# Kernel tuning notes

Hardware: AMD Instinct MI355X
Metric: run time of the kernel (lower is better)

The kernel has to match this reference:

```python
import jax, jax.numpy as jnp
import numpy as np

B, S, D = 2, 2048, 1024
H, HD = 16, 64  # num_attention_heads, attention_head_size


def setup_inputs() -> dict:
    key = jax.random.key(0)
    ks = jax.random.split(key, 8)
    std = 0.02
    return {
        "hidden_states": jax.random.normal(ks[0], (B, S, D), dtype=jnp.float32),
        "attention_mask": jnp.zeros((B, 1, 1, S), dtype=jnp.float32),
        "Wq": jax.random.normal(ks[1], (D, D), dtype=jnp.float32) * std,
        "bq": jnp.zeros((D,), dtype=jnp.float32),
        "Wk": jax.random.normal(ks[2], (D, D), dtype=jnp.float32) * std,
        "bk": jnp.zeros((D,), dtype=jnp.float32),
        "Wv": jax.random.normal(ks[3], (D, D), dtype=jnp.float32) * std,
        "bv": jnp.zeros((D,), dtype=jnp.float32),
    }


def reference(hidden_states, attention_mask, Wq, bq, Wk, bk, Wv, bv):
    b, s, d = hidden_states.shape

    def split_heads(x):  # [b,s,D] -> [b,H,s,HD]
        return x.reshape(b, s, H, HD).transpose(0, 2, 1, 3)

    q = split_heads(hidden_states @ Wq + bq)
    k = split_heads(hidden_states @ Wk + bk)
    v = split_heads(hidden_states @ Wv + bv)

    scores = jnp.einsum("bhqd,bhkd->bhqk", q, k) / jnp.sqrt(jnp.float32(HD))
    scores = scores + attention_mask  # additive mask, broadcast [b,1,1,s]
    probs = jax.nn.softmax(scores, axis=-1)  # dropout is identity at inference
    ctx = jnp.einsum("bhqk,bhkd->bhqd", probs, v)
    out = ctx.transpose(0, 2, 1, 3).reshape(b, s, d)
    return out
```

## Files before the change

### kernel.cpp

```cpp
#include <hip/hip_runtime.h>
#include <math.h>

#define CB 2
#define CS 2048
#define CD 1024
#define CH 16
#define CHD 64
#define CM (CB*CS)

#define QSCALE 0.18033688f
#define LOG2E  1.44269504f
#define BLOG   40.0f

typedef unsigned short u16;
using bf16x8 = __attribute__((ext_vector_type(8))) short;
using u16x8  = __attribute__((ext_vector_type(8))) unsigned short;
using f32x4  = __attribute__((ext_vector_type(4))) float;

__device__ __forceinline__ u16 f2bf(float f) {
    unsigned int u = __float_as_uint(f);
    u = (u + 0x7FFFu + ((u >> 16) & 1u)) >> 16;
    return (u16)u;
}

__device__ __forceinline__ unsigned pack2bf(float a, float b) {
    unsigned ua = (__float_as_uint(a) + 0x8000u) >> 16;
    unsigned ub = (__float_as_uint(b) + 0x8000u) & 0xFFFF0000u;
    return ua | ub;
}

__device__ __forceinline__ void load_lds16(const u16* g, u16* l) {
    __builtin_amdgcn_global_load_lds(
        (const __attribute__((address_space(1))) unsigned int*)g,
        (__attribute__((address_space(3))) unsigned int*)l, 16, 0, 0);
}

__global__ __launch_bounds__(256)
void convert_x(const float* __restrict__ X, u16* __restrict__ Xb)
{
    size_t i = ((size_t)blockIdx.x * 256 + threadIdx.x) * 8;
    float4 v0 = *(const float4*)(X + i);
    float4 v1 = *(const float4*)(X + i + 4);
    u16x8 o;
    o[0] = f2bf(v0.x); o[1] = f2bf(v0.y); o[2] = f2bf(v0.z); o[3] = f2bf(v0.w);
    o[4] = f2bf(v1.x); o[5] = f2bf(v1.y); o[6] = f2bf(v1.z); o[7] = f2bf(v1.w);
    *(u16x8*)(Xb + i) = o;
}

__global__ __launch_bounds__(256)
void convert_wt(const float* __restrict__ Wq, const float* __restrict__ Wk,
                const float* __restrict__ Wv, u16* __restrict__ Wt)
{
    const int z = blockIdx.z;
    const float* W = (z == 0) ? Wq : (z == 1) ? Wk : Wv;
    const float sc = (z == 0) ? QSCALE : 1.0f;
    u16* Wo = Wt + (size_t)z * CD * CD;

    __shared__ u16 T[64][72];
    const int k0 = blockIdx.x << 6;
    const int n0 = blockIdx.y << 6;
    const int tid = threadIdx.x;

    #pragma unroll
    for (int it = 0; it < 4; ++it) {
        int r = (tid >> 4) + (it << 4);
        int c = (tid & 15) << 2;
        float4 v = *(const float4*)(W + (size_t)(k0 + r) * CD + n0 + c);
        T[c + 0][r] = f2bf(v.x * sc);
        T[c + 1][r] = f2bf(v.y * sc);
        T[c + 2][r] = f2bf(v.z * sc);
        T[c + 3][r] = f2bf(v.w * sc);
    }
    __syncthreads();
    #pragma unroll
    for (int it = 0; it < 2; ++it) {
        int cc = tid + (it << 8);
        int n  = cc >> 3;
        int ch = (cc & 7) << 3;
        *(uint4*)(Wo + (size_t)(n0 + n) * CD + k0 + ch) = *(const uint4*)&T[n][ch];
    }
}

__global__ __launch_bounds__(256, 3)
void qkv_gemm_mfma(const u16* __restrict__ Xb, const u16* __restrict__ Wt,
                   const float* __restrict__ bq, const float* __restrict__ bk,
                   const float* __restrict__ bv,
                   u16* __restrict__ Qb, u16* __restrict__ Kb,
                   u16* __restrict__ Vt)
{
    const int z = blockIdx.z;
    const u16* W = Wt + (size_t)z * CD * CD;
    const float* bias = (z == 0) ? bq : (z == 1) ? bk : bv;
    const float bscale = (z == 0) ? QSCALE : 1.0f;

    __shared__ u16 smem[16384];
    u16* As = smem;
    u16* Bs = smem + 8192;

    const int tid  = threadIdx.x;
    const int w    = tid >> 6;
    const int l    = tid & 63;
    const int l15  = l & 15;
    const int quad = l >> 4;
    const int wm   = w >> 1;
    const int wn   = w & 1;

    const int row0 = blockIdx.x << 7;
    const int n0   = blockIdx.y << 7;

    f32x4 acc[4][4];
    #pragma unroll
    for (int mi = 0; mi < 4; ++mi)
        #pragma unroll
        for (int nt = 0; nt < 4; ++nt)
            acc[mi][nt] = (f32x4){0.f, 0.f, 0.f, 0.f};

    const u16* Ag = Xb + (size_t)row0 * CD;
    const u16* Bg = W  + (size_t)n0   * CD;
    const int lr8 = l >> 3;
    const int ls  = l & 7;
    const int lg  = (ls ^ lr8) << 3;
    const int q7  = l15 & 7;

    for (int k0 = 0; k0 < CD; k0 += 64) {
        __syncthreads();
        #pragma unroll
        for (int i = 0; i < 4; ++i) {
            int r = w * 32 + 8 * i + lr8;
            load_lds16(Ag + (size_t)r * CD + k0 + lg, As + (size_t)(w * 32 + 8 * i) * 64);
            load_lds16(Bg + (size_t)r * CD + k0 + lg, Bs + (size_t)(w * 32 + 8 * i) * 64);
        }
        __syncthreads();

        #pragma unroll
        for (int kk = 0; kk < 2; ++kk) {
            bf16x8 af[4], bfr[4];
            #pragma unroll
            for (int mi = 0; mi < 4; ++mi)
                af[mi] = *(const bf16x8*)
                    &As[(wm * 64 + mi * 16 + l15) * 64 + (((kk * 4 + quad) ^ q7) << 3)];
            #pragma unroll
            for (int nt = 0; nt < 4; ++nt)
                bfr[nt] = *(const bf16x8*)
                    &Bs[(wn * 64 + nt * 16 + l15) * 64 + (((kk * 4 + quad) ^ q7) << 3)];
            #pragma unroll
            for (int mi = 0; mi < 4; ++mi)
                #pragma unroll
                for (int nt = 0; nt < 4; ++nt)
                    acc[mi][nt] = __builtin_amdgcn_mfma_f32_16x16x32_bf16(
                        af[mi], bfr[nt], acc[mi][nt], 0, 0, 0);
        }
    }

    __syncthreads();

    if (z < 2) {
        u16* Og = (z == 0) ? Qb : Kb;
        float bb[4];
        #pragma unroll
        for (int nt = 0; nt < 4; ++nt)
            bb[nt] = bias[n0 + wn * 64 + nt * 16 + l15] * bscale;

        u16 (*Ct)[136] = (u16(*)[136])smem;
        #pragma unroll
        for (int mh = 0; mh < 2; ++mh) {
            if (wm == mh) {
                #pragma unroll
                for (int nt = 0; nt < 4; ++nt)
                    #pragma unroll
                    for (int mi = 0; mi < 4; ++mi)
                        #pragma unroll
                        for (int r = 0; r < 4; ++r)
                            Ct[mi * 16 + quad * 4 + r][wn * 64 + nt * 16 + l15] =
                                f2bf(acc[mi][nt][r] + bb[nt]);
            }
            __syncthreads();
            #pragma unroll
            for (int it = 0; it < 4; ++it) {
                int c  = tid + (it << 8);
                int rl = c >> 4;
                int ck = c & 15;
                uint4 d = *(const uint4*)&Ct[rl][ck * 8];
                int gcol = n0 + ck * 8;
                int h = gcol >> 6, hd = gcol & 63;
                int m = row0 + mh * 64 + rl;
                int b = m >> 11, s = m & (CS - 1);
                *(uint4*)(Og + ((size_t)(b * CH + h) * CS + s) * CHD + hd) = d;
            }
            __syncthreads();
        }
    } else {
        u16 (*Ct)[136] = (u16(*)[136])smem;
        #pragma unroll
        for (int nh = 0; nh < 2; ++nh) {
            if (wn == nh) {
                #pragma unroll
                for (int nt = 0; nt < 4; ++nt) {
                    int col = n0 + nh * 64 + nt * 16 + l15;
                    float bb = bias[col];
                    #pragma unroll
                    for (int mi = 0; mi < 4; ++mi)
                        #pragma unroll
                        for (int r = 0; r < 4; ++r) {
                            int ml = wm * 64 + mi * 16 + quad * 4 + r;
                            Ct[nt * 16 + l15][ml] = f2bf(acc[mi][nt][r] + bb);
                        }
                }
            }
            __syncthreads();
            #pragma unroll
            for (int it = 0; it < 4; ++it) {
                int c   = tid + (it << 8);
                int dvl = c >> 4;
                int ch  = c & 15;
                uint4 vdat = *(const uint4*)&Ct[dvl][ch * 8];
                int col = n0 + nh * 64 + dvl;
                int h   = col >> 6;
                int dv  = col & 63;
                int m0  = row0 + ch * 8;
                int b   = m0 >> 11;
                int s0  = m0 & (CS - 1);
                *(uint4*)(Vt + (((size_t)(b * CH + h)) * CHD + dv) * CS + s0) = vdat;
            }
            __syncthreads();
        }
    }
}

__global__ __launch_bounds__(256, 2)
void attn_mfma(const u16* __restrict__ Qg, const u16* __restrict__ Kg,
               const u16* __restrict__ Vtg, const float* __restrict__ mask,
               float* __restrict__ out)
{
    __shared__ float msk[CS];
    __shared__ u16   Kst[2][64 * 64];
    __shared__ u16   Vst[2][64 * 64];
    __shared__ u16   Pl[4][32 * 64];
    __shared__ float abuf[4][32];

    const int q0  = blockIdx.x << 7;
    const int bh  = blockIdx.y;
    const int b   = bh >> 4;
    const int h   = bh & 15;
    const int tid = threadIdx.x;
    const int w    = tid >> 6;
    const int l    = tid & 63;
    const int l15  = l & 15;
    const int quad = l >> 4;
    const int q7   = l15 & 7;
    const int lr8  = l >> 3;
    const int lg   = ((l & 7) ^ lr8) << 3;

    const u16* Qp = Qg  + (size_t)bh * CS * CHD;
    const u16* Kp = Kg  + (size_t)bh * CS * CHD;
    const u16* Vp = Vtg + (size_t)bh * CHD * CS;
    const float* mrow = mask + (size_t)b * CS;

    {
        int i = tid * 8;
        float4 a = *(const float4*)(mrow + i);
        float4 c = *(const float4*)(mrow + i + 4);
        msk[i + 0] = a.x * LOG2E - BLOG; msk[i + 1] = a.y * LOG2E - BLOG;
        msk[i + 2] = a.z * LOG2E - BLOG; msk[i + 3] = a.w * LOG2E - BLOG;
        msk[i + 4] = c.x * LOG2E - BLOG; msk[i + 5] = c.y * LOG2E - BLOG;
        msk[i + 6] = c.z * LOG2E - BLOG; msk[i + 7] = c.w * LOG2E - BLOG;
    }

    auto stage = [&](int k0, int bb) {
        #pragma unroll
        for (int i = 0; i < 2; ++i) {
            int rl = w * 16 + 8 * i;
            load_lds16(Kp + (size_t)(k0 + rl + lr8) * CHD + lg, &Kst[bb][rl * 64]);
            load_lds16(Vp + (size_t)(rl + lr8) * CS + k0 + lg,  &Vst[bb][rl * 64]);
        }
    };

    stage(0, 0);

    bf16x8 qf[2][2];
    #pragma unroll
    for (int nq = 0; nq < 2; ++nq)
        #pragma unroll
        for (int hh = 0; hh < 2; ++hh)
            qf[nq][hh] = *(const bf16x8*)(
                Qp + (size_t)(q0 + w * 32 + nq * 16 + l15) * CHD + hh * 32 + quad * 8);

    u16* Pw = &Pl[w][0];
    float lsum[2] = {0.f, 0.f};
    f32x4 O[2][4];
    #pragma unroll
    for (int nq = 0; nq < 2; ++nq)
        #pragma unroll
        for (int dt = 0; dt < 4; ++dt)
            O[nq][dt] = (f32x4){0.f, 0.f, 0.f, 0.f};

    for (int kt = 0; kt < CS / 64; ++kt) {
        const int k0 = kt << 6;
        const int cc = kt & 1;
        __syncthreads();
        if (kt + 1 < CS / 64)
            stage(k0 + 64, cc ^ 1);

        bf16x8 kf[4][2];
        #pragma unroll
        for (int mt = 0; mt < 4; ++mt)
            #pragma unroll
            for (int hh = 0; hh < 2; ++hh)
                kf[mt][hh] = *(const bf16x8*)
                    &Kst[cc][(mt * 16 + l15) * 64 + (((hh * 4 + quad) ^ q7) << 3)];

        #pragma unroll
        for (int nq = 0; nq < 2; ++nq) {
            f32x4 st[4];
            #pragma unroll
            for (int mt = 0; mt < 4; ++mt) {
                f32x4 c0 = *(const f32x4*)&msk[k0 + mt * 16 + quad * 4];
                c0 = __builtin_amdgcn_mfma_f32_16x16x32_bf16(kf[mt][0], qf[nq][0], c0, 0, 0, 0);
                st[mt] = __builtin_amdgcn_mfma_f32_16x16x32_bf16(kf[mt][1], qf[nq][1], c0, 0, 0, 0);
            }
            float rs = lsum[nq];
            #pragma unroll
            for (int mt = 0; mt < 4; ++mt) {
                #pragma unroll
                for (int r = 0; r < 4; ++r) {
                    st[mt][r] = exp2f(st[mt][r]);
                    rs += st[mt][r];
                }
                int g = 2 * mt + (quad >> 1);
                int addr = (nq * 16 + l15) * 64 + ((g ^ q7) << 3) + ((quad & 1) << 2);
                uint2 d;
                d.x = pack2bf(st[mt][0], st[mt][1]);
                d.y = pack2bf(st[mt][2], st[mt][3]);
                *(uint2*)&Pw[addr] = d;
            }
            lsum[nq] = rs;
        }

        bf16x8 pf[2][2];
        #pragma unroll
        for (int nq = 0; nq < 2; ++nq)
            #pragma unroll
            for (int hh = 0; hh < 2; ++hh)
                pf[nq][hh] = *(const bf16x8*)
                    &Pw[(nq * 16 + l15) * 64 + (((hh * 4 + quad) ^ q7) << 3)];

        bf16x8 vf[4][2];
        #pragma unroll
        for (int dt = 0; dt < 4; ++dt)
            #pragma unroll
            for (int hh = 0; hh < 2; ++hh)
                vf[dt][hh] = *(const bf16x8*)
                    &Vst[cc][(dt * 16 + l15) * 64 + (((hh * 4 + quad) ^ q7) << 3)];

        #pragma unroll
        for (int nq = 0; nq < 2; ++nq)
            #pragma unroll
            for (int dt = 0; dt < 4; ++dt) {
                O[nq][dt] = __builtin_amdgcn_mfma_f32_16x16x32_bf16(
                    pf[nq][0], vf[dt][0], O[nq][dt], 0, 0, 0);
                O[nq][dt] = __builtin_amdgcn_mfma_f32_16x16x32_bf16(
                    pf[nq][1], vf[dt][1], O[nq][dt], 0, 0, 0);
            }
    }

    #pragma unroll
    for (int nq = 0; nq < 2; ++nq) {
        lsum[nq] += __shfl_xor(lsum[nq], 16);
        lsum[nq] += __shfl_xor(lsum[nq], 32);
    }
    if (quad == 0) {
        abuf[w][l15]      = lsum[0];
        abuf[w][16 + l15] = lsum[1];
    }
    __builtin_amdgcn_s_waitcnt(0);

    #pragma unroll
    for (int nq = 0; nq < 2; ++nq) {
        f32x4 lo = *(const f32x4*)&abuf[w][nq * 16 + quad * 4];
        #pragma unroll
        for (int r = 0; r < 4; ++r) {
            float inv = 1.0f / lo[r];
            int q = q0 + w * 32 + nq * 16 + quad * 4 + r;
            float* orow = out + ((size_t)b * CS + q) * CD + h * CHD;
            #pragma unroll
            for (int dt = 0; dt < 4; ++dt)
                orow[dt * 16 + l15] = O[nq][dt][r] * inv;
        }
    }
}

extern "C" void kernel_launch(void* const* d_in, const int* in_sizes, int n_in,
                              void* d_out, int out_size, void* d_ws, size_t ws_size,
                              hipStream_t stream)
{
    const float* X    = (const float*)d_in[0];
    const float* mask = (const float*)d_in[1];
    const float* Wq   = (const float*)d_in[2];
    const float* bq   = (const float*)d_in[3];
    const float* Wk   = (const float*)d_in[4];
    const float* bk   = (const float*)d_in[5];
    const float* Wv   = (const float*)d_in[6];
    const float* bv   = (const float*)d_in[7];
    float* out = (float*)d_out;

    char* ws = (char*)d_ws;
    u16* Xb = (u16*)(ws);
    u16* Wt = (u16*)(ws + ((size_t)8  << 20));
    u16* Qb = (u16*)(ws + ((size_t)14 << 20));
    u16* Kb = (u16*)(ws + ((size_t)22 << 20));
    u16* Vt = (u16*)(ws + ((size_t)30 << 20));

    convert_x<<<CM * CD / (256 * 8), 256, 0, stream>>>(X, Xb);
    convert_wt<<<dim3(16, 16, 3), 256, 0, stream>>>(Wq, Wk, Wv, Wt);
    qkv_gemm_mfma<<<dim3(CM / 128, CD / 128, 3), 256, 0, stream>>>(
        Xb, Wt, bq, bk, bv, Qb, Kb, Vt);
    attn_mfma<<<dim3(CS / 128, CB * CH), 256, 0, stream>>>(Qb, Kb, Vt, mask, out);
}
```

Baseline: 194.7 us.

## Shrink GEMM and attention tiles to raise occupancy and block count

The QKV GEMM tile goes from 128x128 to 128x64 output, with the grid reordered so blocks sharing a row panel of X are adjacent, and launch bounds raised. The attention kernel drops from 128 to 64 queries per block (16 per wave), removes K/V double buffering and the LDS row-sum buffer, and targets 4 blocks per CU. Smaller tiles cut register and LDS use so more waves can run, but they add load traffic per FLOP and remove the prefetch overlap in attention.

```diff
diff --git a/kernel.cpp b/kernel.cpp
--- a/kernel.cpp
+++ b/kernel.cpp
@@ -81,7 +81,7 @@
     }
 }
 
-__global__ __launch_bounds__(256, 3)
+__global__ __launch_bounds__(256, 6)
 void qkv_gemm_mfma(const u16* __restrict__ Xb, const u16* __restrict__ Wt,
                    const float* __restrict__ bq, const float* __restrict__ bk,
                    const float* __restrict__ bv,
@@ -93,7 +93,7 @@
     const float* bias = (z == 0) ? bq : (z == 1) ? bk : bv;
     const float bscale = (z == 0) ? QSCALE : 1.0f;
 
-    __shared__ u16 smem[16384];
+    __shared__ u16 smem[12288];
     u16* As = smem;
     u16* Bs = smem + 8192;
 
@@ -105,140 +105,123 @@
     const int wm   = w >> 1;
     const int wn   = w & 1;
 
-    const int row0 = blockIdx.x << 7;
-    const int n0   = blockIdx.y << 7;
-
-    f32x4 acc[4][4];
+    const int n0   = blockIdx.x << 6;
+    const int row0 = blockIdx.y << 7;
+
+    f32x4 acc[4][2];
     #pragma unroll
     for (int mi = 0; mi < 4; ++mi)
         #pragma unroll
-        for (int nt = 0; nt < 4; ++nt)
+        for (int nt = 0; nt < 2; ++nt)
             acc[mi][nt] = (f32x4){0.f, 0.f, 0.f, 0.f};
 
     const u16* Ag = Xb + (size_t)row0 * CD;
     const u16* Bg = W  + (size_t)n0   * CD;
     const int lr8 = l >> 3;
-    const int ls  = l & 7;
-    const int lg  = (ls ^ lr8) << 3;
+    const int lg  = ((l & 7) ^ lr8) << 3;
     const int q7  = l15 & 7;
 
     for (int k0 = 0; k0 < CD; k0 += 64) {
         __syncthreads();
         #pragma unroll
         for (int i = 0; i < 4; ++i) {
-            int r = w * 32 + 8 * i + lr8;
-            load_lds16(Ag + (size_t)r * CD + k0 + lg, As + (size_t)(w * 32 + 8 * i) * 64);
-            load_lds16(Bg + (size_t)r * CD + k0 + lg, Bs + (size_t)(w * 32 + 8 * i) * 64);
+            int r = w * 32 + 8 * i;
+            load_lds16(Ag + (size_t)(r + lr8) * CD + k0 + lg, As + (size_t)r * 64);
+        }
+        #pragma unroll
+        for (int i = 0; i < 2; ++i) {
+            int r = w * 16 + 8 * i;
+            load_lds16(Bg + (size_t)(r + lr8) * CD + k0 + lg, Bs + (size_t)r * 64);
         }
         __syncthreads();
 
         #pragma unroll
         for (int kk = 0; kk < 2; ++kk) {
-            bf16x8 af[4], bfr[4];
+            const int slot = ((kk * 4 + quad) ^ q7) << 3;
+            bf16x8 af[4], bfr[2];
             #pragma unroll
             for (int mi = 0; mi < 4; ++mi)
-                af[mi] = *(const bf16x8*)
-                    &As[(wm * 64 + mi * 16 + l15) * 64 + (((kk * 4 + quad) ^ q7) << 3)];
-            #pragma unroll
-            for (int nt = 0; nt < 4; ++nt)
-                bfr[nt] = *(const bf16x8*)
-                    &Bs[(wn * 64 + nt * 16 + l15) * 64 + (((kk * 4 + quad) ^ q7) << 3)];
+                af[mi] = *(const bf16x8*)&As[(wm * 64 + mi * 16 + l15) * 64 + slot];
+            #pragma unroll
+            for (int nt = 0; nt < 2; ++nt)
+                bfr[nt] = *(const bf16x8*)&Bs[(wn * 32 + nt * 16 + l15) * 64 + slot];
             #pragma unroll
             for (int mi = 0; mi < 4; ++mi)
                 #pragma unroll
-                for (int nt = 0; nt < 4; ++nt)
+                for (int nt = 0; nt < 2; ++nt)
                     acc[mi][nt] = __builtin_amdgcn_mfma_f32_16x16x32_bf16(
                         af[mi], bfr[nt], acc[mi][nt], 0, 0, 0);
         }
     }
 
     __syncthreads();
+    const int h = n0 >> 6;
 
     if (z < 2) {
         u16* Og = (z == 0) ? Qb : Kb;
-        float bb[4];
-        #pragma unroll
-        for (int nt = 0; nt < 4; ++nt)
-            bb[nt] = bias[n0 + wn * 64 + nt * 16 + l15] * bscale;
-
-        u16 (*Ct)[136] = (u16(*)[136])smem;
-        #pragma unroll
-        for (int mh = 0; mh < 2; ++mh) {
-            if (wm == mh) {
+        float bb[2];
+        #pragma unroll
+        for (int nt = 0; nt < 2; ++nt)
+            bb[nt] = bias[n0 + wn * 32 + nt * 16 + l15] * bscale;
+
+        u16 (*Ct)[72] = (u16(*)[72])smem;
+        #pragma unroll
+        for (int nt = 0; nt < 2; ++nt)
+            #pragma unroll
+            for (int mi = 0; mi < 4; ++mi)
                 #pragma unroll
-                for (int nt = 0; nt < 4; ++nt)
-                    #pragma unroll
-                    for (int mi = 0; mi < 4; ++mi)
-                        #pragma unroll
-                        for (int r = 0; r < 4; ++r)
-                            Ct[mi * 16 + quad * 4 + r][wn * 64 + nt * 16 + l15] =
-                                f2bf(acc[mi][nt][r] + bb[nt]);
-            }
-            __syncthreads();
-            #pragma unroll
-            for (int it = 0; it < 4; ++it) {
-                int c  = tid + (it << 8);
-                int rl = c >> 4;
-                int ck = c & 15;
-                uint4 d = *(const uint4*)&Ct[rl][ck * 8];
-                int gcol = n0 + ck * 8;
-                int h = gcol >> 6, hd = gcol & 63;
-                int m = row0 + mh * 64 + rl;
-                int b = m >> 11, s = m & (CS - 1);
-                *(uint4*)(Og + ((size_t)(b * CH + h) * CS + s) * CHD + hd) = d;
-            }
-            __syncthreads();
+                for (int r = 0; r < 4; ++r)
+                    Ct[wm * 64 + mi * 16 + quad * 4 + r][wn * 32 + nt * 16 + l15] =
+                        f2bf(acc[mi][nt][r] + bb[nt]);
+        __syncthreads();
+        #pragma unroll
+        for (int it = 0; it < 4; ++it) {
+            int c  = tid + (it << 8);
+            int rl = c >> 3;
+            int ck = c & 7;
+            uint4 d = *(const uint4*)&Ct[rl][ck * 8];
+            int m = row0 + rl;
+            int b = m >> 11, s = m & (CS - 1);
+            *(uint4*)(Og + ((size_t)(b * CH + h) * CS + s) * CHD + ck * 8) = d;
         }
     } else {
         u16 (*Ct)[136] = (u16(*)[136])smem;
         #pragma unroll
-        for (int nh = 0; nh < 2; ++nh) {
-            if (wn == nh) {
+        for (int nt = 0; nt < 2; ++nt) {
+            float bb = bias[n0 + wn * 32 + nt * 16 + l15];
+            #pragma unroll
+            for (int mi = 0; mi < 4; ++mi)
                 #pragma unroll
-                for (int nt = 0; nt < 4; ++nt) {
-                    int col = n0 + nh * 64 + nt * 16 + l15;
-                    float bb = bias[col];
-                    #pragma unroll
-                    for (int mi = 0; mi < 4; ++mi)
-                        #pragma unroll
-                        for (int r = 0; r < 4; ++r) {
-                            int ml = wm * 64 + mi * 16 + quad * 4 + r;
-                            Ct[nt * 16 + l15][ml] = f2bf(acc[mi][nt][r] + bb);
-                        }
-                }
-            }
-            __syncthreads();
-            #pragma unroll
-            for (int it = 0; it < 4; ++it) {
-                int c   = tid + (it << 8);
-                int dvl = c >> 4;
-                int ch  = c & 15;
-                uint4 vdat = *(const uint4*)&Ct[dvl][ch * 8];
-                int col = n0 + nh * 64 + dvl;
-                int h   = col >> 6;
-                int dv  = col & 63;
-                int m0  = row0 + ch * 8;
-                int b   = m0 >> 11;
-                int s0  = m0 & (CS - 1);
-                *(uint4*)(Vt + (((size_t)(b * CH + h)) * CHD + dv) * CS + s0) = vdat;
-            }
-            __syncthreads();
-        }
-    }
-}
-
-__global__ __launch_bounds__(256, 2)
+                for (int r = 0; r < 4; ++r)
+                    Ct[wn * 32 + nt * 16 + l15][wm * 64 + mi * 16 + quad * 4 + r] =
+                        f2bf(acc[mi][nt][r] + bb);
+        }
+        __syncthreads();
+        #pragma unroll
+        for (int it = 0; it < 4; ++it) {
+            int c   = tid + (it << 8);
+            int dvl = c >> 4;
+            int ch  = c & 15;
+            uint4 vdat = *(const uint4*)&Ct[dvl][ch * 8];
+            int m0 = row0 + ch * 8;
+            int b  = m0 >> 11;
+            int s0 = m0 & (CS - 1);
+            *(uint4*)(Vt + (((size_t)(b * CH + h)) * CHD + dvl) * CS + s0) = vdat;
+        }
+    }
+}
+
+__global__ __launch_bounds__(256, 4)
 void attn_mfma(const u16* __restrict__ Qg, const u16* __restrict__ Kg,
                const u16* __restrict__ Vtg, const float* __restrict__ mask,
                float* __restrict__ out)
 {
     __shared__ float msk[CS];
-    __shared__ u16   Kst[2][64 * 64];
-    __shared__ u16   Vst[2][64 * 64];
-    __shared__ u16   Pl[4][32 * 64];
-    __shared__ float abuf[4][32];
-
-    const int q0  = blockIdx.x << 7;
+    __shared__ u16   Kst[64 * 64];
+    __shared__ u16   Vst[64 * 64];
+    __shared__ u16   Pl[4][16 * 64];
+
+    const int q0  = blockIdx.x << 6;
     const int bh  = blockIdx.y;
     const int b   = bh >> 4;
     const int h   = bh & 15;
@@ -266,40 +249,28 @@
         msk[i + 6] = c.z * LOG2E - BLOG; msk[i + 7] = c.w * LOG2E - BLOG;
     }
 
-    auto stage = [&](int k0, int bb) {
+    bf16x8 qf[2];
+    #pragma unroll
+    for (int hh = 0; hh < 2; ++hh)
+        qf[hh] = *(const bf16x8*)(
+            Qp + (size_t)(q0 + w * 16 + l15) * CHD + hh * 32 + quad * 8);
+
+    u16* Pw = &Pl[w][0];
+    float lsum = 0.f;
+    f32x4 O[4];
+    #pragma unroll
+    for (int dt = 0; dt < 4; ++dt) O[dt] = (f32x4){0.f, 0.f, 0.f, 0.f};
+
+    for (int kt = 0; kt < CS / 64; ++kt) {
+        const int k0 = kt << 6;
+        __syncthreads();
         #pragma unroll
         for (int i = 0; i < 2; ++i) {
             int rl = w * 16 + 8 * i;
-            load_lds16(Kp + (size_t)(k0 + rl + lr8) * CHD + lg, &Kst[bb][rl * 64]);
-            load_lds16(Vp + (size_t)(rl + lr8) * CS + k0 + lg,  &Vst[bb][rl * 64]);
-        }
-    };
-
-    stage(0, 0);
-
-    bf16x8 qf[2][2];
-    #pragma unroll
-    for (int nq = 0; nq < 2; ++nq)
-        #pragma unroll
-        for (int hh = 0; hh < 2; ++hh)
-            qf[nq][hh] = *(const bf16x8*)(
-                Qp + (size_t)(q0 + w * 32 + nq * 16 + l15) * CHD + hh * 32 + quad * 8);
-
-    u16* Pw = &Pl[w][0];
-    float lsum[2] = {0.f, 0.f};
-    f32x4 O[2][4];
-    #pragma unroll
-    for (int nq = 0; nq < 2; ++nq)
-        #pragma unroll
-        for (int dt = 0; dt < 4; ++dt)
-            O[nq][dt] = (f32x4){0.f, 0.f, 0.f, 0.f};
-
-    for (int kt = 0; kt < CS / 64; ++kt) {
-        const int k0 = kt << 6;
-        const int cc = kt & 1;
-        __syncthreads();
-        if (kt + 1 < CS / 64)
-            stage(k0 + 64, cc ^ 1);
+            load_lds16(Kp + (size_t)(k0 + rl + lr8) * CHD + lg, &Kst[rl * 64]);
+            load_lds16(Vp + (size_t)(rl + lr8) * CS + k0 + lg,  &Vst[rl * 64]);
+        }
+        __syncthreads();
 
         bf16x8 kf[4][2];
         #pragma unroll
@@ -307,42 +278,38 @@
             #pragma unroll
             for (int hh = 0; hh < 2; ++hh)
                 kf[mt][hh] = *(const bf16x8*)
-                    &Kst[cc][(mt * 16 + l15) * 64 + (((hh * 4 + quad) ^ q7) << 3)];
-
-        #pragma unroll
-        for (int nq = 0; nq < 2; ++nq) {
-            f32x4 st[4];
-            #pragma unroll
-            for (int mt = 0; mt < 4; ++mt) {
-                f32x4 c0 = *(const f32x4*)&msk[k0 + mt * 16 + quad * 4];
-                c0 = __builtin_amdgcn_mfma_f32_16x16x32_bf16(kf[mt][0], qf[nq][0], c0, 0, 0, 0);
-                st[mt] = __builtin_amdgcn_mfma_f32_16x16x32_bf16(kf[mt][1], qf[nq][1], c0, 0, 0, 0);
+                    &Kst[(mt * 16 + l15) * 64 + (((hh * 4 + quad) ^ q7) << 3)];
+
+        f32x4 st[4];
+        #pragma unroll
+        for (int mt = 0; mt < 4; ++mt) {
+            f32x4 c0 = *(const f32x4*)&msk[k0 + mt * 16 + quad * 4];
+            c0 = __builtin_amdgcn_mfma_f32_16x16x32_bf16(kf[mt][0], qf[0], c0, 0, 0, 0);
+            st[mt] = __builtin_amdgcn_mfma_f32_16x16x32_bf16(kf[mt][1], qf[1], c0, 0, 0, 0);
+        }
+
+        float rs = lsum;
+        #pragma unroll
+        for (int mt = 0; mt < 4; ++mt) {
+            #pragma unroll
+            for (int r = 0; r < 4; ++r) {
+                st[mt][r] = exp2f(st[mt][r]);
+                rs += st[mt][r];
             }
-            float rs = lsum[nq];
-            #pragma unroll
-            for (int mt = 0; mt < 4; ++mt) {
-                #pragma unroll
-                for (int r = 0; r < 4; ++r) {
-                    st[mt][r] = exp2f(st[mt][r]);
-                    rs += st[mt][r];
-                }
-                int g = 2 * mt + (quad >> 1);
-                int addr = (nq * 16 + l15) * 64 + ((g ^ q7) << 3) + ((quad & 1) << 2);
-                uint2 d;
-                d.x = pack2bf(st[mt][0], st[mt][1]);
-                d.y = pack2bf(st[mt][2], st[mt][3]);
-                *(uint2*)&Pw[addr] = d;
-            }
-            lsum[nq] = rs;
-        }
-
-        bf16x8 pf[2][2];
-        #pragma unroll
-        for (int nq = 0; nq < 2; ++nq)
-            #pragma unroll
-            for (int hh = 0; hh < 2; ++hh)
-                pf[nq][hh] = *(const bf16x8*)
-                    &Pw[(nq * 16 + l15) * 64 + (((hh * 4 + quad) ^ q7) << 3)];
+            int g = 2 * mt + (quad >> 1);
+            int addr = l15 * 64 + ((g ^ q7) << 3) + ((quad & 1) << 2);
+            uint2 d;
+            d.x = pack2bf(st[mt][0], st[mt][1]);
+            d.y = pack2bf(st[mt][2], st[mt][3]);
+            *(uint2*)&Pw[addr] = d;
+        }
+        lsum = rs;
+
+        bf16x8 pf[2];
+        #pragma unroll
+        for (int hh = 0; hh < 2; ++hh)
+            pf[hh] = *(const bf16x8*)
+                &Pw[l15 * 64 + (((hh * 4 + quad) ^ q7) << 3)];
 
         bf16x8 vf[4][2];
         #pragma unroll
@@ -350,42 +317,26 @@
             #pragma unroll
             for (int hh = 0; hh < 2; ++hh)
                 vf[dt][hh] = *(const bf16x8*)
-                    &Vst[cc][(dt * 16 + l15) * 64 + (((hh * 4 + quad) ^ q7) << 3)];
-
-        #pragma unroll
-        for (int nq = 0; nq < 2; ++nq)
-            #pragma unroll
-            for (int dt = 0; dt < 4; ++dt) {
-                O[nq][dt] = __builtin_amdgcn_mfma_f32_16x16x32_bf16(
-                    pf[nq][0], vf[dt][0], O[nq][dt], 0, 0, 0);
-                O[nq][dt] = __builtin_amdgcn_mfma_f32_16x16x32_bf16(
-                    pf[nq][1], vf[dt][1], O[nq][dt], 0, 0, 0);
-            }
-    }
-
-    #pragma unroll
-    for (int nq = 0; nq < 2; ++nq) {
-        lsum[nq] += __shfl_xor(lsum[nq], 16);
-        lsum[nq] += __shfl_xor(lsum[nq], 32);
-    }
-    if (quad == 0) {
-        abuf[w][l15]      = lsum[0];
-        abuf[w][16 + l15] = lsum[1];
-    }
-    __builtin_amdgcn_s_waitcnt(0);
-
-    #pragma unroll
-    for (int nq = 0; nq < 2; ++nq) {
-        f32x4 lo = *(const f32x4*)&abuf[w][nq * 16 + quad * 4];
-        #pragma unroll
-        for (int r = 0; r < 4; ++r) {
-            float inv = 1.0f / lo[r];
-            int q = q0 + w * 32 + nq * 16 + quad * 4 + r;
-            float* orow = out + ((size_t)b * CS + q) * CD + h * CHD;
-            #pragma unroll
-            for (int dt = 0; dt < 4; ++dt)
-                orow[dt * 16 + l15] = O[nq][dt][r] * inv;
-        }
+                    &Vst[(dt * 16 + l15) * 64 + (((hh * 4 + quad) ^ q7) << 3)];
+
+        #pragma unroll
+        for (int dt = 0; dt < 4; ++dt) {
+            O[dt] = __builtin_amdgcn_mfma_f32_16x16x32_bf16(pf[0], vf[dt][0], O[dt], 0, 0, 0);
+            O[dt] = __builtin_amdgcn_mfma_f32_16x16x32_bf16(pf[1], vf[dt][1], O[dt], 0, 0, 0);
+        }
+    }
+
+    lsum += __shfl_xor(lsum, 16);
+    lsum += __shfl_xor(lsum, 32);
+
+    #pragma unroll
+    for (int r = 0; r < 4; ++r) {
+        float inv = 1.0f / __shfl(lsum, quad * 4 + r);
+        int q = q0 + w * 16 + quad * 4 + r;
+        float* orow = out + ((size_t)b * CS + q) * CD + h * CHD;
+        #pragma unroll
+        for (int dt = 0; dt < 4; ++dt)
+            orow[dt * 16 + l15] = O[dt][r] * inv;
     }
 }
 
@@ -412,7 +363,7 @@
 
     convert_x<<<CM * CD / (256 * 8), 256, 0, stream>>>(X, Xb);
     convert_wt<<<dim3(16, 16, 3), 256, 0, stream>>>(Wq, Wk, Wv, Wt);
-    qkv_gemm_mfma<<<dim3(CM / 128, CD / 128, 3), 256, 0, stream>>>(
+    qkv_gemm_mfma<<<dim3(CD / 64, CM / 128, 3), 256, 0, stream>>>(
         Xb, Wt, bq, bk, bv, Qb, Kb, Vt);
-    attn_mfma<<<dim3(CS / 128, CB * CH), 256, 0, stream>>>(Qb, Kb, Vt, mask, out);
-}
+    attn_mfma<<<dim3(CS / 64, CB * CH), 256, 0, stream>>>(Qb, Kb, Vt, mask, out);
+}
```

Result: slower. 198.8 us (+2.1%).

## Shrink attention tile to 64 queries per block and prefetch mask into registers

Applied to the files above, without the earlier changes.

The attention kernel now handles 16 query rows per wave (64 per block) instead of 32, doubling the grid and raising launch bounds to 4 blocks per SM. The shared mask array and the shared row-sum buffer are removed. Mask values are prefetched from global memory into registers one tile ahead, and the row sums are broadcast with shuffles. This aims to improve occupancy and latency hiding by cutting registers and LDS per block. In exchange, each K/V tile staged into LDS is reused by half as many queries, so K/V traffic doubles.

```diff
diff --git a/kernel.cpp b/kernel.cpp
--- a/kernel.cpp
+++ b/kernel.cpp
@@ -227,18 +227,16 @@
     }
 }
 
-__global__ __launch_bounds__(256, 2)
+__global__ __launch_bounds__(256, 4)
 void attn_mfma(const u16* __restrict__ Qg, const u16* __restrict__ Kg,
                const u16* __restrict__ Vtg, const float* __restrict__ mask,
                float* __restrict__ out)
 {
-    __shared__ float msk[CS];
-    __shared__ u16   Kst[2][64 * 64];
-    __shared__ u16   Vst[2][64 * 64];
-    __shared__ u16   Pl[4][32 * 64];
-    __shared__ float abuf[4][32];
-
-    const int q0  = blockIdx.x << 7;
+    __shared__ u16 Kst[2][64 * 64];
+    __shared__ u16 Vst[2][64 * 64];
+    __shared__ u16 Pl[4][16 * 64];
+
+    const int q0  = blockIdx.x << 6;
     const int bh  = blockIdx.y;
     const int b   = bh >> 4;
     const int h   = bh & 15;
@@ -256,16 +254,6 @@
     const u16* Vp = Vtg + (size_t)bh * CHD * CS;
     const float* mrow = mask + (size_t)b * CS;
 
-    {
-        int i = tid * 8;
-        float4 a = *(const float4*)(mrow + i);
-        float4 c = *(const float4*)(mrow + i + 4);
-        msk[i + 0] = a.x * LOG2E - BLOG; msk[i + 1] = a.y * LOG2E - BLOG;
-        msk[i + 2] = a.z * LOG2E - BLOG; msk[i + 3] = a.w * LOG2E - BLOG;
-        msk[i + 4] = c.x * LOG2E - BLOG; msk[i + 5] = c.y * LOG2E - BLOG;
-        msk[i + 6] = c.z * LOG2E - BLOG; msk[i + 7] = c.w * LOG2E - BLOG;
-    }
-
     auto stage = [&](int k0, int bb) {
         #pragma unroll
         for (int i = 0; i < 2; ++i) {
@@ -277,22 +265,26 @@
 
     stage(0, 0);
 
-    bf16x8 qf[2][2];
-    #pragma unroll
-    for (int nq = 0; nq < 2; ++nq)
-        #pragma unroll
-        for (int hh = 0; hh < 2; ++hh)
-            qf[nq][hh] = *(const bf16x8*)(
-                Qp + (size_t)(q0 + w * 32 + nq * 16 + l15) * CHD + hh * 32 + quad * 8);
+    bf16x8 qf[2];
+    #pragma unroll
+    for (int hh = 0; hh < 2; ++hh)
+        qf[hh] = *(const bf16x8*)(
+            Qp + (size_t)(q0 + w * 16 + l15) * CHD + hh * 32 + quad * 8);
+
+    f32x4 mc[4];
+    #pragma unroll
+    for (int mt = 0; mt < 4; ++mt) {
+        f32x4 mv = *(const f32x4*)(mrow + mt * 16 + quad * 4);
+        #pragma unroll
+        for (int r = 0; r < 4; ++r)
+            mc[mt][r] = fmaf(mv[r], LOG2E, -BLOG);
+    }
 
     u16* Pw = &Pl[w][0];
-    float lsum[2] = {0.f, 0.f};
-    f32x4 O[2][4];
-    #pragma unroll
-    for (int nq = 0; nq < 2; ++nq)
-        #pragma unroll
-        for (int dt = 0; dt < 4; ++dt)
-            O[nq][dt] = (f32x4){0.f, 0.f, 0.f, 0.f};
+    float lsum = 0.f;
+    f32x4 O[4];
+    #pragma unroll
+    for (int dt = 0; dt < 4; ++dt) O[dt] = (f32x4){0.f, 0.f, 0.f, 0.f};
 
     for (int kt = 0; kt < CS / 64; ++kt) {
         const int k0 = kt << 6;
@@ -301,6 +293,17 @@
         if (kt + 1 < CS / 64)
             stage(k0 + 64, cc ^ 1);
 
+        f32x4 mn[4];
+        if (kt + 1 < CS / 64) {
+            #pragma unroll
+            for (int mt = 0; mt < 4; ++mt) {
+                f32x4 mv = *(const f32x4*)(mrow + k0 + 64 + mt * 16 + quad * 4);
+                #pragma unroll
+                for (int r = 0; r < 4; ++r)
+                    mn[mt][r] = fmaf(mv[r], LOG2E, -BLOG);
+            }
+        }
+
         bf16x8 kf[4][2];
         #pragma unroll
         for (int mt = 0; mt < 4; ++mt)
@@ -309,40 +312,36 @@
                 kf[mt][hh] = *(const bf16x8*)
                     &Kst[cc][(mt * 16 + l15) * 64 + (((hh * 4 + quad) ^ q7) << 3)];
 
-        #pragma unroll
-        for (int nq = 0; nq < 2; ++nq) {
-            f32x4 st[4];
-            #pragma unroll
-            for (int mt = 0; mt < 4; ++mt) {
-                f32x4 c0 = *(const f32x4*)&msk[k0 + mt * 16 + quad * 4];
-                c0 = __builtin_amdgcn_mfma_f32_16x16x32_bf16(kf[mt][0], qf[nq][0], c0, 0, 0, 0);
-                st[mt] = __builtin_amdgcn_mfma_f32_16x16x32_bf16(kf[mt][1], qf[nq][1], c0, 0, 0, 0);
-            }
-            float rs = lsum[nq];
-            #pragma unroll
-            for (int mt = 0; mt < 4; ++mt) {
-                #pragma unroll
-                for (int r = 0; r < 4; ++r) {
-                    st[mt][r] = exp2f(st[mt][r]);
-                    rs += st[mt][r];
-                }
-                int g = 2 * mt + (quad >> 1);
-                int addr = (nq * 16 + l15) * 64 + ((g ^ q7) << 3) + ((quad & 1) << 2);
-                uint2 d;
-                d.x = pack2bf(st[mt][0], st[mt][1]);
-                d.y = pack2bf(st[mt][2], st[mt][3]);
-                *(uint2*)&Pw[addr] = d;
-            }
-            lsum[nq] = rs;
-        }
-
-        bf16x8 pf[2][2];
-        #pragma unroll
-        for (int nq = 0; nq < 2; ++nq)
-            #pragma unroll
-            for (int hh = 0; hh < 2; ++hh)
-                pf[nq][hh] = *(const bf16x8*)
-                    &Pw[(nq * 16 + l15) * 64 + (((hh * 4 + quad) ^ q7) << 3)];
+        f32x4 st[4];
+        #pragma unroll
+        for (int mt = 0; mt < 4; ++mt) {
+            f32x4 c0 = mc[mt];
+            c0 = __builtin_amdgcn_mfma_f32_16x16x32_bf16(kf[mt][0], qf[0], c0, 0, 0, 0);
+            st[mt] = __builtin_amdgcn_mfma_f32_16x16x32_bf16(kf[mt][1], qf[1], c0, 0, 0, 0);
+        }
+
+        float rs = lsum;
+        #pragma unroll
+        for (int mt = 0; mt < 4; ++mt) {
+            #pragma unroll
+            for (int r = 0; r < 4; ++r) {
+                st[mt][r] = exp2f(st[mt][r]);
+                rs += st[mt][r];
+            }
+            int g = 2 * mt + (quad >> 1);
+            int addr = l15 * 64 + ((g ^ q7) << 3) + ((quad & 1) << 2);
+            uint2 d;
+            d.x = pack2bf(st[mt][0], st[mt][1]);
+            d.y = pack2bf(st[mt][2], st[mt][3]);
+            *(uint2*)&Pw[addr] = d;
+        }
+        lsum = rs;
+
+        bf16x8 pf[2];
+        #pragma unroll
+        for (int hh = 0; hh < 2; ++hh)
+            pf[hh] = *(const bf16x8*)
+                &Pw[l15 * 64 + (((hh * 4 + quad) ^ q7) << 3)];
 
         bf16x8 vf[4][2];
         #pragma unroll
@@ -353,39 +352,26 @@
                     &Vst[cc][(dt * 16 + l15) * 64 + (((hh * 4 + quad) ^ q7) << 3)];
 
         #pragma unroll
-        for (int nq = 0; nq < 2; ++nq)
-            #pragma unroll
-            for (int dt = 0; dt < 4; ++dt) {
-                O[nq][dt] = __builtin_amdgcn_mfma_f32_16x16x32_bf16(
-                    pf[nq][0], vf[dt][0], O[nq][dt], 0, 0, 0);
-                O[nq][dt] = __builtin_amdgcn_mfma_f32_16x16x32_bf16(
-                    pf[nq][1], vf[dt][1], O[nq][dt], 0, 0, 0);
-            }
-    }
-
-    #pragma unroll
-    for (int nq = 0; nq < 2; ++nq) {
-        lsum[nq] += __shfl_xor(lsum[nq], 16);
-        lsum[nq] += __shfl_xor(lsum[nq], 32);
-    }
-    if (quad == 0) {
-        abuf[w][l15]      = lsum[0];
-        abuf[w][16 + l15] = lsum[1];
-    }
-    __builtin_amdgcn_s_waitcnt(0);
-
-    #pragma unroll
-    for (int nq = 0; nq < 2; ++nq) {
-        f32x4 lo = *(const f32x4*)&abuf[w][nq * 16 + quad * 4];
-        #pragma unroll
-        for (int r = 0; r < 4; ++r) {
-            float inv = 1.0f / lo[r];
-            int q = q0 + w * 32 + nq * 16 + quad * 4 + r;
-            float* orow = out + ((size_t)b * CS + q) * CD + h * CHD;
-            #pragma unroll
-            for (int dt = 0; dt < 4; ++dt)
-                orow[dt * 16 + l15] = O[nq][dt][r] * inv;
-        }
+        for (int dt = 0; dt < 4; ++dt) {
+            O[dt] = __builtin_amdgcn_mfma_f32_16x16x32_bf16(pf[0], vf[dt][0], O[dt], 0, 0, 0);
+            O[dt] = __builtin_amdgcn_mfma_f32_16x16x32_bf16(pf[1], vf[dt][1], O[dt], 0, 0, 0);
+        }
+
+        #pragma unroll
+        for (int mt = 0; mt < 4; ++mt) mc[mt] = mn[mt];
+    }
+
+    lsum += __shfl_xor(lsum, 16);
+    lsum += __shfl_xor(lsum, 32);
+
+    #pragma unroll
+    for (int r = 0; r < 4; ++r) {
+        float inv = 1.0f / __shfl(lsum, quad * 4 + r);
+        int q = q0 + w * 16 + quad * 4 + r;
+        float* orow = out + ((size_t)b * CS + q) * CD + h * CHD;
+        #pragma unroll
+        for (int dt = 0; dt < 4; ++dt)
+            orow[dt * 16 + l15] = O[dt][r] * inv;
     }
 }
 
@@ -414,5 +400,5 @@
     convert_wt<<<dim3(16, 16, 3), 256, 0, stream>>>(Wq, Wk, Wv, Wt);
     qkv_gemm_mfma<<<dim3(CM / 128, CD / 128, 3), 256, 0, stream>>>(
         Xb, Wt, bq, bk, bv, Qb, Kb, Vt);
-    attn_mfma<<<dim3(CS / 128, CB * CH), 256, 0, stream>>>(Qb, Kb, Vt, mask, out);
-}
+    attn_mfma<<<dim3(CS / 64, CB * CH), 256, 0, stream>>>(Qb, Kb, Vt, mask, out);
+}
```

Result: no change. 194.2 us (-0.3%).
